# Kernel optimization log

Hardware: AMD Instinct MI355X
Metric: run time of the kernel (lower is better)

## Reference

```python
import jax, jax.numpy as jnp
import numpy as np

BLOCK = 8  # block size N from init_kwargs


def _dct_basis(N):
    x = jnp.arange(N, dtype=jnp.float32)[:, None]
    u = jnp.arange(N, dtype=jnp.float32)[None, :]
    alpha = jnp.full((N,), jnp.sqrt(2.0 / N), dtype=jnp.float32).at[0].set(jnp.sqrt(1.0 / N))
    D = alpha[None, :] * jnp.cos(jnp.pi * u * (2.0 * x + 1.0) / (2.0 * N))  # [x, u]
    # 2D separable basis: basis[x, y, u, v] = D[x, u] * D[y, v]
    return D[:, None, :, None] * D[None, :, None, :]


def _corner_masks(N):
    mid = N // 2
    m = jnp.zeros((4, N, N), dtype=jnp.float32)
    m = m.at[0, :mid, :mid].set(1.0)
    m = m.at[1, :mid, mid:].set(1.0)
    m = m.at[2, mid:, :mid].set(1.0)
    m = m.at[3, mid:, mid:].set(1.0)
    return m


def setup_inputs() -> dict:
    key = jax.random.key(0)
    x = jax.random.normal(key, (32, 3, 512, 512), dtype=jnp.float32)
    return {"x": x}


def reference(x):
    N = BLOCK
    basis = _dct_basis(N)          # [N, N, N, N] -> (x, y, u, v)
    masks = _corner_masks(N)       # [4, N, N]
    b, d, h, w = x.shape
    nh, nw = h // N, w // N
    # tile image into (b, d, nh, nw, N, N) blocks
    blocks = x.reshape(b, d, nh, N, nw, N).transpose(0, 1, 2, 4, 3, 5)
    # forward block DCT: contract spatial (i, j) against basis -> frequency (k, l)
    coeffs = jnp.einsum('bdhwij,ijkl->bdhwkl', blocks, basis)
    # apply 4 corner masks -> (4, b, d, nh, nw, N, N)
    corner = coeffs[None] * masks[:, None, None, None, None]
    # inverse block DCT: contract frequency (k, l) against basis -> spatial (i, j)
    imgs = jnp.einsum('cbdhwkl,ijkl->cbdhwij', corner, basis)
    # un-tile: (4, b, d, nh, N, nw, N) -> (4, b, d, h, w)
    return imgs.transpose(0, 1, 2, 3, 5, 4, 6).reshape(4, b, d, h, w)
```

## Files before the change

kernel.cpp:

```cpp
#include <hip/hip_runtime.h>

__device__ __constant__ static const float kD[8][8] = {
  { 0.3535533906f,  0.4903926402f,  0.4619397663f,  0.4157348062f,  0.3535533906f,  0.2777851165f,  0.1913417162f,  0.0975451610f},
  { 0.3535533906f,  0.4157348062f,  0.1913417162f, -0.0975451610f, -0.3535533906f, -0.4903926402f, -0.4619397663f, -0.2777851165f},
  { 0.3535533906f,  0.2777851165f, -0.1913417162f, -0.4903926402f, -0.3535533906f,  0.0975451610f,  0.4619397663f,  0.4157348062f},
  { 0.3535533906f,  0.0975451610f, -0.4619397663f, -0.2777851165f,  0.3535533906f,  0.4157348062f, -0.1913417162f, -0.4903926402f},
  { 0.3535533906f, -0.0975451610f, -0.4619397663f,  0.2777851165f,  0.3535533906f, -0.4157348062f, -0.1913417162f,  0.4903926402f},
  { 0.3535533906f, -0.2777851165f, -0.1913417162f,  0.4903926402f, -0.3535533906f, -0.0975451610f,  0.4619397663f, -0.4157348062f},
  { 0.3535533906f, -0.4157348062f,  0.1913417162f,  0.0975451610f, -0.3535533906f,  0.4903926402f, -0.4619397663f,  0.2777851165f},
  { 0.3535533906f, -0.4903926402f,  0.4619397663f, -0.4157348062f,  0.3535533906f, -0.2777851165f,  0.1913417162f, -0.0975451610f},
};

#define NPLANES   96
#define IMG_W     512
#define PLANE_SZ  (512 * 512)
#define NBLOCKS   (NPLANES * 64 * 64)

__global__ __launch_bounds__(256) void dct_corners_kernel(
    const float* __restrict__ x, float* __restrict__ out) {
  const int g = blockIdx.x * 256 + threadIdx.x;
  if (g >= NBLOCKS) return;

  const int p   = g >> 12;
  const int blk = g & 4095;
  const int by  = blk >> 6;
  const int bx  = blk & 63;

  const size_t base = (size_t)p * PLANE_SZ + (size_t)(by * 8) * IMG_W + (size_t)(bx * 8);
  const float* src = x + base;

  float s[8][8];
#pragma unroll
  for (int r = 0; r < 8; ++r) {
    const float4 a = *reinterpret_cast<const float4*>(src + r * IMG_W);
    const float4 b = *reinterpret_cast<const float4*>(src + r * IMG_W + 4);
    s[r][0] = a.x; s[r][1] = a.y; s[r][2] = a.z; s[r][3] = a.w;
    s[r][4] = b.x; s[r][5] = b.y; s[r][6] = b.z; s[r][7] = b.w;
  }

  float V[8][8];
#pragma unroll
  for (int u = 0; u < 8; ++u) {
#pragma unroll
    for (int j = 0; j < 8; ++j) {
      float acc = 0.0f;
#pragma unroll
      for (int r = 0; r < 8; ++r) acc = fmaf(kD[r][u], s[r][j], acc);
      V[u][j] = acc;
    }
  }

  float C[8][8];
#pragma unroll
  for (int k = 0; k < 8; ++k) {
#pragma unroll
    for (int l = 0; l < 8; ++l) {
      float acc = 0.0f;
#pragma unroll
      for (int j = 0; j < 8; ++j) acc = fmaf(V[k][j], kD[j][l], acc);
      C[k][l] = acc;
    }
  }

  float TL[8][8], TH[8][8];
#pragma unroll
  for (int k = 0; k < 8; ++k) {
#pragma unroll
    for (int j = 0; j < 8; ++j) {
      float al = 0.0f, ah = 0.0f;
#pragma unroll
      for (int l = 0; l < 4; ++l) {
        al = fmaf(C[k][l],     kD[j][l],     al);
        ah = fmaf(C[k][l + 4], kD[j][l + 4], ah);
      }
      TL[k][j] = al;
      TH[k][j] = ah;
    }
  }

  const size_t corner_stride = (size_t)NPLANES * PLANE_SZ;
  float* o = out + base;
#pragma unroll
  for (int i = 0; i < 8; ++i) {
    float r0[8], r1[8], r2[8], r3[8];
#pragma unroll
    for (int j = 0; j < 8; ++j) {
      float a0 = 0.0f, a1 = 0.0f, a2 = 0.0f, a3 = 0.0f;
#pragma unroll
      for (int k = 0; k < 4; ++k) {
        const float dl = kD[i][k];
        const float dh = kD[i][k + 4];
        a0 = fmaf(dl, TL[k][j],     a0);
        a1 = fmaf(dl, TH[k][j],     a1);
        a2 = fmaf(dh, TL[k + 4][j], a2);
        a3 = fmaf(dh, TH[k + 4][j], a3);
      }
      r0[j] = a0; r1[j] = a1; r2[j] = a2; r3[j] = a3;
    }
    float* row = o + (size_t)i * IMG_W;
    *reinterpret_cast<float4*>(row)                         = make_float4(r0[0], r0[1], r0[2], r0[3]);
    *reinterpret_cast<float4*>(row + 4)                     = make_float4(r0[4], r0[5], r0[6], r0[7]);
    *reinterpret_cast<float4*>(row + corner_stride)         = make_float4(r1[0], r1[1], r1[2], r1[3]);
    *reinterpret_cast<float4*>(row + corner_stride + 4)     = make_float4(r1[4], r1[5], r1[6], r1[7]);
    *reinterpret_cast<float4*>(row + 2 * corner_stride)     = make_float4(r2[0], r2[1], r2[2], r2[3]);
    *reinterpret_cast<float4*>(row + 2 * corner_stride + 4) = make_float4(r2[4], r2[5], r2[6], r2[7]);
    *reinterpret_cast<float4*>(row + 3 * corner_stride)     = make_float4(r3[0], r3[1], r3[2], r3[3]);
    *reinterpret_cast<float4*>(row + 3 * corner_stride + 4) = make_float4(r3[4], r3[5], r3[6], r3[7]);
  }
}

extern "C" void kernel_launch(void* const* d_in, const int* in_sizes, int n_in,
                              void* d_out, int out_size, void* d_ws, size_t ws_size,
                              hipStream_t stream) {
  const float* x = (const float*)d_in[0];
  float* out = (float*)d_out;
  const int threads = 256;
  const int grid = (NBLOCKS + threads - 1) / threads;
  hipLaunchKernelGGL(dct_corners_kernel, dim3(grid), dim3(threads), 0, stream, x, out);
}
```

Before: 485.6 us.

## Replace DCT round-trip with precomputed low-pass projection and split blocks across lane pairs

Folds the forward DCT, the corner masking and the inverse DCT into a single precomputed 8x8 projection matrix G = D_low*D_low^T. Each corner output is computed as G*X*G or from complements (X - ...), which cuts the four separate inverse transforms down to a few small matrix products. Each 8x8 block is now split across two threads, each holding four mirrored rows. The threads exchange partner rows with a cross-half lane shuffle, so per-thread register pressure drops and thread count doubles. The approach relies on the symmetric structure of G and the complement identities, and the hardcoded constants carry float rounding error.

New measurement: 466.1 us. 4.0% less time.

```diff
diff --git a/kernel.cpp b/kernel.cpp
--- a/kernel.cpp
+++ b/kernel.cpp
@@ -1,111 +1,99 @@
 #include <hip/hip_runtime.h>
 
-__device__ __constant__ static const float kD[8][8] = {
-  { 0.3535533906f,  0.4903926402f,  0.4619397663f,  0.4157348062f,  0.3535533906f,  0.2777851165f,  0.1913417162f,  0.0975451610f},
-  { 0.3535533906f,  0.4157348062f,  0.1913417162f, -0.0975451610f, -0.3535533906f, -0.4903926402f, -0.4619397663f, -0.2777851165f},
-  { 0.3535533906f,  0.2777851165f, -0.1913417162f, -0.4903926402f, -0.3535533906f,  0.0975451610f,  0.4619397663f,  0.4157348062f},
-  { 0.3535533906f,  0.0975451610f, -0.4619397663f, -0.2777851165f,  0.3535533906f,  0.4157348062f, -0.1913417162f, -0.4903926402f},
-  { 0.3535533906f, -0.0975451610f, -0.4619397663f,  0.2777851165f,  0.3535533906f, -0.4157348062f, -0.1913417162f,  0.4903926402f},
-  { 0.3535533906f, -0.2777851165f, -0.1913417162f,  0.4903926402f, -0.3535533906f, -0.0975451610f,  0.4619397663f, -0.4157348062f},
-  { 0.3535533906f, -0.4157348062f,  0.1913417162f,  0.0975451610f, -0.3535533906f,  0.4903926402f, -0.4619397663f,  0.2777851165f},
-  { 0.3535533906f, -0.4903926402f,  0.4619397663f, -0.4157348062f,  0.3535533906f, -0.2777851165f,  0.1913417162f, -0.0975451610f},
+constexpr float kG[8][8] = {
+  { 0.7517087183f,  0.3767087182f, -0.0310378601f, -0.1560378601f, -0.0207388351f,  0.1042611649f,  0.0500679770f, -0.0749320231f},
+  { 0.3767087182f,  0.3439621399f,  0.2517087183f,  0.1042611649f, -0.0310378601f, -0.0749320231f, -0.0207388351f,  0.0500679770f},
+  {-0.0310378601f,  0.2517087183f,  0.4792611650f,  0.3767087182f,  0.0500679770f, -0.1560378602f, -0.0749320231f,  0.1042611649f},
+  {-0.1560378601f,  0.1042611649f,  0.3767087182f,  0.4250679770f,  0.2517087182f,  0.0500679770f, -0.0310378601f, -0.0207388351f},
+  {-0.0207388351f, -0.0310378601f,  0.0500679770f,  0.2517087182f,  0.4250679770f,  0.3767087182f,  0.1042611649f, -0.1560378601f},
+  { 0.1042611649f, -0.0749320231f, -0.1560378602f,  0.0500679770f,  0.3767087182f,  0.4792611650f,  0.2517087183f, -0.0310378601f},
+  { 0.0500679770f, -0.0207388351f, -0.0749320231f, -0.0310378601f,  0.1042611649f,  0.2517087183f,  0.3439621399f,  0.3767087182f},
+  {-0.0749320231f,  0.0500679770f,  0.1042611649f, -0.0207388351f, -0.1560378601f, -0.0310378601f,  0.3767087182f,  0.7517087183f},
 };
 
 #define NPLANES   96
 #define IMG_W     512
 #define PLANE_SZ  (512 * 512)
 #define NBLOCKS   (NPLANES * 64 * 64)
+#define NTHREADS  (NBLOCKS * 2)
 
 __global__ __launch_bounds__(256) void dct_corners_kernel(
     const float* __restrict__ x, float* __restrict__ out) {
-  const int g = blockIdx.x * 256 + threadIdx.x;
-  if (g >= NBLOCKS) return;
+  const int tid  = blockIdx.x * 256 + threadIdx.x;
+  const int lane = threadIdx.x & 63;
+  const int half = lane >> 5;
+  const int bi   = ((tid >> 6) << 5) + (lane & 31);
+  const int p    = bi >> 12;
+  const int blk  = bi & 4095;
+  const int by   = blk >> 6;
+  const int bx   = blk & 63;
 
-  const int p   = g >> 12;
-  const int blk = g & 4095;
-  const int by  = blk >> 6;
-  const int bx  = blk & 63;
+  const size_t pb = (size_t)p * PLANE_SZ + (size_t)(by * 8) * IMG_W + (size_t)(bx * 8);
+  const float* src = x + pb;
 
-  const size_t base = (size_t)p * PLANE_SZ + (size_t)(by * 8) * IMG_W + (size_t)(bx * 8);
-  const float* src = x + base;
-
-  float s[8][8];
+  float s[4][8];
 #pragma unroll
-  for (int r = 0; r < 8; ++r) {
-    const float4 a = *reinterpret_cast<const float4*>(src + r * IMG_W);
-    const float4 b = *reinterpret_cast<const float4*>(src + r * IMG_W + 4);
+  for (int r = 0; r < 4; ++r) {
+    const int ra = half ? (7 - r) : r;
+    const float4 a = *reinterpret_cast<const float4*>(src + (size_t)ra * IMG_W);
+    const float4 c = *reinterpret_cast<const float4*>(src + (size_t)ra * IMG_W + 4);
     s[r][0] = a.x; s[r][1] = a.y; s[r][2] = a.z; s[r][3] = a.w;
-    s[r][4] = b.x; s[r][5] = b.y; s[r][6] = b.z; s[r][7] = b.w;
+    s[r][4] = c.x; s[r][5] = c.y; s[r][6] = c.z; s[r][7] = c.w;
   }
 
-  float V[8][8];
+  float A[4][8];
 #pragma unroll
-  for (int u = 0; u < 8; ++u) {
+  for (int j = 0; j < 8; ++j) {
+    const float o0 = __shfl_xor(s[0][j], 32, 64);
+    const float o1 = __shfl_xor(s[1][j], 32, 64);
+    const float o2 = __shfl_xor(s[2][j], 32, 64);
+    const float o3 = __shfl_xor(s[3][j], 32, 64);
 #pragma unroll
-    for (int j = 0; j < 8; ++j) {
-      float acc = 0.0f;
-#pragma unroll
-      for (int r = 0; r < 8; ++r) acc = fmaf(kD[r][u], s[r][j], acc);
-      V[u][j] = acc;
+    for (int i = 0; i < 4; ++i) {
+      float acc =      kG[i][0] * s[0][j];
+      acc = fmaf(kG[i][1], s[1][j], acc);
+      acc = fmaf(kG[i][2], s[2][j], acc);
+      acc = fmaf(kG[i][3], s[3][j], acc);
+      acc = fmaf(kG[i][4], o3, acc);
+      acc = fmaf(kG[i][5], o2, acc);
+      acc = fmaf(kG[i][6], o1, acc);
+      acc = fmaf(kG[i][7], o0, acc);
+      A[i][j] = acc;
     }
   }
 
-  float C[8][8];
+  const size_t CS = (size_t)NPLANES * PLANE_SZ;
+  float* od = out + pb;
 #pragma unroll
-  for (int k = 0; k < 8; ++k) {
+  for (int i = 0; i < 4; ++i) {
+    const int ra = half ? (7 - i) : i;
+    float* row = od + (size_t)ra * IMG_W;
+
+    float bv[8];
 #pragma unroll
-    for (int l = 0; l < 8; ++l) {
-      float acc = 0.0f;
-#pragma unroll
-      for (int j = 0; j < 8; ++j) acc = fmaf(V[k][j], kD[j][l], acc);
-      C[k][l] = acc;
-    }
-  }
+    for (int j = 0; j < 8; ++j) bv[j] = s[i][j] - A[i][j];
 
-  float TL[8][8], TH[8][8];
-#pragma unroll
-  for (int k = 0; k < 8; ++k) {
+    float t0[8], t2[8];
 #pragma unroll
     for (int j = 0; j < 8; ++j) {
-      float al = 0.0f, ah = 0.0f;
+      float aA = A[i][0] * kG[0][j];
+      float aB = bv[0]   * kG[0][j];
 #pragma unroll
-      for (int l = 0; l < 4; ++l) {
-        al = fmaf(C[k][l],     kD[j][l],     al);
-        ah = fmaf(C[k][l + 4], kD[j][l + 4], ah);
+      for (int l = 1; l < 8; ++l) {
+        aA = fmaf(A[i][l], kG[l][j], aA);
+        aB = fmaf(bv[l],   kG[l][j], aB);
       }
-      TL[k][j] = al;
-      TH[k][j] = ah;
+      t0[j] = aA; t2[j] = aB;
     }
-  }
 
-  const size_t corner_stride = (size_t)NPLANES * PLANE_SZ;
-  float* o = out + base;
-#pragma unroll
-  for (int i = 0; i < 8; ++i) {
-    float r0[8], r1[8], r2[8], r3[8];
-#pragma unroll
-    for (int j = 0; j < 8; ++j) {
-      float a0 = 0.0f, a1 = 0.0f, a2 = 0.0f, a3 = 0.0f;
-#pragma unroll
-      for (int k = 0; k < 4; ++k) {
-        const float dl = kD[i][k];
-        const float dh = kD[i][k + 4];
-        a0 = fmaf(dl, TL[k][j],     a0);
-        a1 = fmaf(dl, TH[k][j],     a1);
-        a2 = fmaf(dh, TL[k + 4][j], a2);
-        a3 = fmaf(dh, TH[k + 4][j], a3);
-      }
-      r0[j] = a0; r1[j] = a1; r2[j] = a2; r3[j] = a3;
-    }
-    float* row = o + (size_t)i * IMG_W;
-    *reinterpret_cast<float4*>(row)                         = make_float4(r0[0], r0[1], r0[2], r0[3]);
-    *reinterpret_cast<float4*>(row + 4)                     = make_float4(r0[4], r0[5], r0[6], r0[7]);
-    *reinterpret_cast<float4*>(row + corner_stride)         = make_float4(r1[0], r1[1], r1[2], r1[3]);
-    *reinterpret_cast<float4*>(row + corner_stride + 4)     = make_float4(r1[4], r1[5], r1[6], r1[7]);
-    *reinterpret_cast<float4*>(row + 2 * corner_stride)     = make_float4(r2[0], r2[1], r2[2], r2[3]);
-    *reinterpret_cast<float4*>(row + 2 * corner_stride + 4) = make_float4(r2[4], r2[5], r2[6], r2[7]);
-    *reinterpret_cast<float4*>(row + 3 * corner_stride)     = make_float4(r3[0], r3[1], r3[2], r3[3]);
-    *reinterpret_cast<float4*>(row + 3 * corner_stride + 4) = make_float4(r3[4], r3[5], r3[6], r3[7]);
+    *reinterpret_cast<float4*>(row)              = make_float4(t0[0], t0[1], t0[2], t0[3]);
+    *reinterpret_cast<float4*>(row + 4)          = make_float4(t0[4], t0[5], t0[6], t0[7]);
+    *reinterpret_cast<float4*>(row + CS)         = make_float4(A[i][0] - t0[0], A[i][1] - t0[1], A[i][2] - t0[2], A[i][3] - t0[3]);
+    *reinterpret_cast<float4*>(row + CS + 4)     = make_float4(A[i][4] - t0[4], A[i][5] - t0[5], A[i][6] - t0[6], A[i][7] - t0[7]);
+    *reinterpret_cast<float4*>(row + 2 * CS)     = make_float4(t2[0], t2[1], t2[2], t2[3]);
+    *reinterpret_cast<float4*>(row + 2 * CS + 4) = make_float4(t2[4], t2[5], t2[6], t2[7]);
+    *reinterpret_cast<float4*>(row + 3 * CS)     = make_float4(bv[0] - t2[0], bv[1] - t2[1], bv[2] - t2[2], bv[3] - t2[3]);
+    *reinterpret_cast<float4*>(row + 3 * CS + 4) = make_float4(bv[4] - t2[4], bv[5] - t2[5], bv[6] - t2[6], bv[7] - t2[7]);
   }
 }
 
@@ -115,6 +103,6 @@
   const float* x = (const float*)d_in[0];
   float* out = (float*)d_out;
   const int threads = 256;
-  const int grid = (NBLOCKS + threads - 1) / threads;
+  const int grid = NTHREADS / threads;
   hipLaunchKernelGGL(dct_corners_kernel, dim3(grid), dim3(threads), 0, stream, x, out);
 }
```
